# Kernel tuning notes

Measured on AMD Instinct MI355X. Metric: run time of the kernel, lower is better.

The kernel has to match this reference:

```python
import jax, jax.numpy as jnp
import numpy as np

D_MODEL = 1024
N_HEADS = 16
HEAD_DIM = D_MODEL // N_HEADS


def setup_inputs() -> dict:
    key = jax.random.key(0)
    k_x, k_qkv, k_out = jax.random.split(key, 3)
    x = jax.random.normal(k_x, (4, 2048, D_MODEL), dtype=jnp.float32)
    # nn.Linear weights are (out_features, in_features); init std=0.02
    w_qkv = jax.random.normal(k_qkv, (3 * D_MODEL, D_MODEL), dtype=jnp.float32) * 0.02
    w_out = jax.random.normal(k_out, (D_MODEL, D_MODEL), dtype=jnp.float32) * 0.02
    return {"x": x, "w_qkv": w_qkv, "w_out": w_out}


def reference(x, w_qkv, w_out):
    B, T, C = x.shape
    H, Dh = N_HEADS, HEAD_DIM
    # qkv projection: x @ w_qkv.T -> (B, T, 3C)
    qkv = jnp.einsum('btc,oc->bto', x, w_qkv)
    q, k, v = jnp.split(qkv, 3, axis=-1)

    def split_heads(t):
        return t.reshape(B, T, H, Dh).transpose(0, 2, 1, 3)  # (B, H, T, Dh)

    q, k, v = split_heads(q), split_heads(k), split_heads(v)
    scale = jnp.sqrt(jnp.asarray(Dh, dtype=x.dtype))
    scores = jnp.einsum('bhqd,bhkd->bhqk', q, k) / scale  # (B, H, T, T)
    causal = jnp.tril(jnp.ones((T, T), dtype=bool))
    scores = jnp.where(causal[None, None], scores, jnp.asarray(-jnp.inf, dtype=scores.dtype))
    attn = jax.nn.softmax(scores, axis=-1)
    out = jnp.einsum('bhqk,bhkd->bhqd', attn, v)  # (B, H, T, Dh)
    out = out.transpose(0, 2, 1, 3).reshape(B, T, C)
    return jnp.einsum('btc,oc->bto', out, w_out)
```

## Files before the change

kernel.cpp:

```cpp
#include <hip/hip_runtime.h>

typedef __attribute__((ext_vector_type(8))) short bf16x8;
typedef __attribute__((ext_vector_type(4))) float f32x4;
typedef __attribute__((ext_vector_type(16))) float f32x16;
typedef __attribute__((ext_vector_type(4))) int i32x4;
using u16 = unsigned short;

constexpr int Bsz = 4, T = 2048, C = 1024, H = 16, Dh = 64;
constexpr int Mrows = Bsz * T;
constexpr int K_DIM = 1024;
constexpr float QSCALE = 0.18033688011112042f;

__device__ inline u16 f2bf(float f) {
    unsigned u = __builtin_bit_cast(unsigned, f);
    u += 0x7FFFu + ((u >> 16) & 1u);
    return (u16)(u >> 16);
}

__device__ inline void g2l16(const void* g, void* l) {
    __builtin_amdgcn_global_load_lds((const __attribute__((address_space(1))) void*)g,
                                     (__attribute__((address_space(3))) void*)l, 16, 0, 0);
}

__device__ inline unsigned pk2(float lo, float hi) {
    unsigned d;
    asm("v_cvt_pk_bf16_f32 %0, %1, %2" : "=v"(d) : "v"(lo), "v"(hi));
    return d;
}
__device__ inline void swap32(unsigned& a, unsigned& b) {
    asm("v_permlane32_swap_b32 %0, %1" : "+v"(a), "+v"(b));
}

__global__ __launch_bounds__(256)
void cvt_k(const float* __restrict__ x, const float* __restrict__ wq,
           const float* __restrict__ wo, u16* __restrict__ xb,
           u16* __restrict__ wqb, u16* __restrict__ wob)
{
    int idx = blockIdx.x * 256 + threadIdx.x;
    const float* src; u16* dst; int rel;
    if (idx < 1048576)      { src = x;  dst = xb;  rel = idx; }
    else if (idx < 1441792) { src = wq; dst = wqb; rel = idx - 1048576; }
    else                    { src = wo; dst = wob; rel = idx - 1441792; }
    size_t off = (size_t)rel * 8;
    float4 a = *(const float4*)(src + off);
    float4 b = *(const float4*)(src + off + 4);
    unsigned r0 = (unsigned)f2bf(a.x) | ((unsigned)f2bf(a.y) << 16);
    unsigned r1 = (unsigned)f2bf(a.z) | ((unsigned)f2bf(a.w) << 16);
    unsigned r2 = (unsigned)f2bf(b.x) | ((unsigned)f2bf(b.y) << 16);
    unsigned r3 = (unsigned)f2bf(b.z) | ((unsigned)f2bf(b.w) << 16);
    *(uint4*)(dst + off) = make_uint4(r0, r1, r2, r3);
}

__device__ inline void stage_g(u16* lds, const u16* gb, int ldg, int tid) {
    #pragma unroll
    for (int i = 0; i < 4; ++i) {
        int ch = i * 256 + tid;
        int r = ch >> 3, c8 = ch & 7;
        int sc = c8 ^ (r & 7);
        g2l16(gb + (size_t)r * ldg + sc * 8, lds + (i * 256 + (tid & 192)) * 8);
    }
}

template<int MODE>
__device__ __forceinline__
void gemm_body(const u16* __restrict__ Ab, const u16* __restrict__ Bb,
               float* __restrict__ Op, u16* __restrict__ qws,
               u16* __restrict__ kws, u16* __restrict__ vtws,
               u16* As, u16* Bs, int m0, int n0)
{
    const int tid = threadIdx.x;
    const int l = tid & 63, wid = tid >> 6;
    const int wm = wid >> 1, wn = wid & 1;
    const int lane16 = l & 15, lhi = l >> 4;

    const u16* Abase = Ab + (size_t)m0 * K_DIM;
    const u16* Bbase = Bb + (size_t)n0 * K_DIM;

    f32x4 acc[4][4] = {};

    for (int ks = 0; ks < K_DIM / 64; ++ks) {
        __syncthreads();
        stage_g(As, Abase + ks * 64, K_DIM, tid);
        stage_g(Bs, Bbase + ks * 64, K_DIM, tid);
        __syncthreads();
        #pragma unroll
        for (int kc = 0; kc < 2; kc++) {
            bf16x8 af[4], bfr[4];
            #pragma unroll
            for (int mi = 0; mi < 4; mi++) {
                int row = wm * 64 + mi * 16 + lane16;
                int byte = row * 128 + kc * 64 + lhi * 16; byte ^= (row & 7) << 4;
                af[mi] = *(const bf16x8*)((const char*)As + byte);
            }
            #pragma unroll
            for (int ni = 0; ni < 4; ni++) {
                int row = wn * 64 + ni * 16 + lane16;
                int byte = row * 128 + kc * 64 + lhi * 16; byte ^= (row & 7) << 4;
                bfr[ni] = *(const bf16x8*)((const char*)Bs + byte);
            }
            #pragma unroll
            for (int mi = 0; mi < 4; mi++)
                #pragma unroll
                for (int ni = 0; ni < 4; ni++) {
                    if constexpr (MODE == 2)
                        acc[mi][ni] = __builtin_amdgcn_mfma_f32_16x16x32_bf16(
                            bfr[ni], af[mi], acc[mi][ni], 0, 0, 0);
                    else
                        acc[mi][ni] = __builtin_amdgcn_mfma_f32_16x16x32_bf16(
                            af[mi], bfr[ni], acc[mi][ni], 0, 0, 0);
                }
        }
    }

    if constexpr (MODE == 2) {
        #pragma unroll
        for (int mi = 0; mi < 4; mi++)
            #pragma unroll
            for (int ni = 0; ni < 4; ni++)
                #pragma unroll
                for (int r = 0; r < 4; r++) {
                    int wr = n0 + wn * 64 + ni * 16 + lhi * 4 + r;
                    int tg = m0 + wm * 64 + mi * 16 + lane16;
                    int hh = (wr >> 6) & 15, d = wr & 63;
                    int bb = tg >> 11, tt = tg & 2047;
                    size_t off = (((size_t)bb * H + hh) * Dh + d) * T + tt;
                    vtws[off] = f2bf(acc[mi][ni][r]);
                }
    } else {
        #pragma unroll
        for (int mi = 0; mi < 4; mi++)
            #pragma unroll
            for (int ni = 0; ni < 4; ni++)
                #pragma unroll
                for (int r = 0; r < 4; r++) {
                    int gm = m0 + wm * 64 + mi * 16 + lhi * 4 + r;
                    int gn = n0 + wn * 64 + ni * 16 + lane16;
                    float val = acc[mi][ni][r];
                    if constexpr (MODE == 0) {
                        int hh = (gn >> 6) & 15, d = gn & 63;
                        int bb = gm >> 11, t = gm & 2047;
                        size_t off = (((size_t)bb * H + hh) * T + t) * Dh + d;
                        if (gn < C) qws[off] = f2bf(val * QSCALE);
                        else        kws[off] = f2bf(val);
                    } else {
                        Op[(size_t)gm * C + gn] = val;
                    }
                }
    }
}

__global__ __launch_bounds__(256)
void gemm_qkv(const u16* __restrict__ xb, const u16* __restrict__ wqkvb,
              u16* __restrict__ qws, u16* __restrict__ kws, u16* __restrict__ vtws)
{
    __shared__ alignas(16) u16 As[128 * 64];
    __shared__ alignas(16) u16 Bs[128 * 64];
    const int m0 = blockIdx.x * 128;
    if (blockIdx.y < 16)
        gemm_body<0>(xb, wqkvb, nullptr, qws, kws, vtws, As, Bs, m0, blockIdx.y * 128);
    else
        gemm_body<2>(xb, wqkvb, nullptr, qws, kws, vtws, As, Bs, m0,
                     2 * C + (blockIdx.y - 16) * 128);
}

__global__ __launch_bounds__(256)
void gemm_out(const u16* __restrict__ ob, const u16* __restrict__ woutb,
              float* __restrict__ Op)
{
    __shared__ alignas(16) u16 As[128 * 64];
    __shared__ alignas(16) u16 Bs[128 * 64];
    gemm_body<1>(ob, woutb, Op, nullptr, nullptr, nullptr, As, Bs,
                 blockIdx.x * 128, blockIdx.y * 128);
}

constexpr float SMAX = 16.0f;

__device__ inline void stage_c(u16* lds, const u16* gb, int rstride, int tid) {
    #pragma unroll
    for (int it = 0; it < 2; ++it) {
        int i = it * 256 + tid;
        int r = i & 63, c8 = i >> 6;
        g2l16(gb + (size_t)r * rstride + c8 * 8, lds + i * 8);
    }
}

__global__ __launch_bounds__(256, 3)
void attn_k(const u16* __restrict__ qws, const u16* __restrict__ kws,
            const u16* __restrict__ vtws, u16* __restrict__ ows)
{
    __shared__ alignas(16) u16 KL[3][64 * 64];
    __shared__ alignas(16) u16 VL[3][64 * 64];

    const int bid = blockIdx.x;
    const int head = bid & 63;
    const int qt = 15 - (bid >> 6);
    const int b = head >> 4, h = head & 15;
    const int tid = threadIdx.x, w = tid >> 6, l = tid & 63;
    const int l31 = l & 31, hi = l >> 5;

    const size_t hoff = (size_t)head * (T * Dh);
    const u16* Qg  = qws + hoff;
    const u16* Kg  = kws + hoff;
    const u16* Vtg = vtws + hoff;

    const int qb = qt * 128;
    const int nt = 2 * qt + 2;
    const int qbw = qb + w * 32;

    bf16x8 qf[4];
    #pragma unroll
    for (int c = 0; c < 4; ++c)
        qf[c] = *(const bf16x8*)(Qg + (size_t)(qbw + l31) * Dh + c * 16 + hi * 8);

    f32x16 o0{}, o1{};
    float lrun = 0.f;

    stage_c(KL[0], Kg, Dh, tid);
    stage_c(VL[0], Vtg, T, tid);
    stage_c(KL[1], Kg + (size_t)64 * Dh, Dh, tid);
    stage_c(VL[1], Vtg + 64, T, tid);

    int cur = 0;
    for (int t = 0; t < nt; ++t) {
        if (t + 1 < nt) asm volatile("s_waitcnt vmcnt(4)" ::: "memory");
        else            asm volatile("s_waitcnt vmcnt(0)" ::: "memory");
        __builtin_amdgcn_s_barrier();
        __builtin_amdgcn_sched_barrier(0);

        int nx = cur + 2; if (nx >= 3) nx -= 3;
        if (t + 2 < nt) {
            stage_c(KL[nx], Kg + (size_t)(t + 2) * 64 * Dh, Dh, tid);
            stage_c(VL[nx], Vtg + (t + 2) * 64, T, tid);
        }

        const int kv0 = t * 64;
        if (kv0 <= qbw + 31) {
            const char* Kb = (const char*)KL[cur];
            const char* Vb = (const char*)VL[cur];

            bf16x8 kf0[4], kf1[4];
            #pragma unroll
            for (int c = 0; c < 4; ++c) {
                int off = (c * 2 + hi) * 1024 + l31 * 16;
                kf0[c] = *(const bf16x8*)(Kb + off);
                kf1[c] = *(const bf16x8*)(Kb + off + 512);
            }

            f32x16 s0{}, s1{};
            #pragma unroll
            for (int c = 0; c < 4; ++c) {
                s0 = __builtin_amdgcn_mfma_f32_32x32x16_bf16(kf0[c], qf[c], s0, 0, 0, 0);
                s1 = __builtin_amdgcn_mfma_f32_32x32x16_bf16(kf1[c], qf[c], s1, 0, 0, 0);
            }

            if (kv0 + 63 > qbw) {
                int qg = qbw + l31;
                #pragma unroll
                for (int r = 0; r < 16; ++r) {
                    int kvg = kv0 + (r & 3) + 8 * (r >> 2) + 4 * hi;
                    if (kvg > qg)      s0[r] = -__builtin_inff();
                    if (kvg + 32 > qg) s1[r] = -__builtin_inff();
                }
            }

            float p0[16], p1[16];
            float t0 = 0.f, t1 = 0.f, t2 = 0.f, t3 = 0.f;
            #pragma unroll
            for (int r = 0; r < 16; ++r) {
                p0[r] = __builtin_amdgcn_exp2f(s0[r] - SMAX);
                p1[r] = __builtin_amdgcn_exp2f(s1[r] - SMAX);
                float s = p0[r] + p1[r];
                if ((r & 3) == 0) t0 += s; else if ((r & 3) == 1) t1 += s;
                else if ((r & 3) == 2) t2 += s; else t3 += s;
            }
            lrun += (t0 + t1) + (t2 + t3);

            unsigned paf[4][4];
            unsigned cc[8];
            #pragma unroll
            for (int i = 0; i < 4; ++i) cc[i]     = pk2(p0[2 * i], p0[2 * i + 1]);
            #pragma unroll
            for (int i = 0; i < 4; ++i) cc[4 + i] = pk2(p0[8 + 2 * i], p0[9 + 2 * i]);
            swap32(cc[0], cc[2]); swap32(cc[1], cc[3]);
            swap32(cc[4], cc[6]); swap32(cc[5], cc[7]);
            #pragma unroll
            for (int i = 0; i < 4; ++i) { paf[0][i] = cc[i]; paf[1][i] = cc[4 + i]; }
            #pragma unroll
            for (int i = 0; i < 4; ++i) cc[i]     = pk2(p1[2 * i], p1[2 * i + 1]);
            #pragma unroll
            for (int i = 0; i < 4; ++i) cc[4 + i] = pk2(p1[8 + 2 * i], p1[9 + 2 * i]);
            swap32(cc[0], cc[2]); swap32(cc[1], cc[3]);
            swap32(cc[4], cc[6]); swap32(cc[5], cc[7]);
            #pragma unroll
            for (int i = 0; i < 4; ++i) { paf[2][i] = cc[i]; paf[3][i] = cc[4 + i]; }

            #pragma unroll
            for (int kb = 0; kb < 4; ++kb) {
                i32x4 wv = {(int)paf[kb][0], (int)paf[kb][1],
                            (int)paf[kb][2], (int)paf[kb][3]};
                bf16x8 pa = __builtin_bit_cast(bf16x8, wv);
                int off = (kb * 2 + hi) * 1024 + l31 * 16;
                bf16x8 v0 = *(const bf16x8*)(Vb + off);
                bf16x8 v1 = *(const bf16x8*)(Vb + off + 512);
                o0 = __builtin_amdgcn_mfma_f32_32x32x16_bf16(pa, v0, o0, 0, 0, 0);
                o1 = __builtin_amdgcn_mfma_f32_32x32x16_bf16(pa, v1, o1, 0, 0, 0);
            }
        }
        cur = (cur == 2) ? 0 : cur + 1;
    }

    float lt = lrun + __shfl_xor(lrun, 32);
    float inv = 1.0f / lt;
    #pragma unroll
    for (int r = 0; r < 16; ++r) {
        int cr = (r & 3) + 8 * (r >> 2) + 4 * hi;
        float il = __shfl(inv, cr);
        size_t rowoff = ((size_t)b * T + qb + w * 32 + cr) * C + h * Dh + l31;
        ows[rowoff]      = f2bf(o0[r] * il);
        ows[rowoff + 32] = f2bf(o1[r] * il);
    }
}

extern "C" void kernel_launch(void* const* d_in, const int* in_sizes, int n_in,
                              void* d_out, int out_size, void* d_ws, size_t ws_size,
                              hipStream_t stream)
{
    const float* x     = (const float*)d_in[0];
    const float* w_qkv = (const float*)d_in[1];
    const float* w_out = (const float*)d_in[2];
    float* out = (float*)d_out;

    const size_t SZ = (size_t)Bsz * H * T * Dh;
    u16* qws   = (u16*)d_ws;
    u16* kws   = qws + SZ;
    u16* vtws  = kws + SZ;
    u16* xb    = vtws + SZ;
    u16* ows   = xb;
    u16* wqkvb = xb + SZ;
    u16* woutb = wqkvb + (size_t)3 * C * C;

    cvt_k<<<dim3(6144), 256, 0, stream>>>(x, w_qkv, w_out, xb, wqkvb, woutb);

    gemm_qkv<<<dim3(Mrows / 128, 24), 256, 0, stream>>>(xb, wqkvb, qws, kws, vtws);

    attn_k<<<dim3(1024), 256, 0, stream>>>(qws, kws, vtws, ows);

    gemm_out<<<dim3(Mrows / 128, C / 128), 256, 0, stream>>>(ows, woutb, out);
}
```

Before: 156.9 us.

## Double-buffer GEMM LDS tiles and raise wave priority around attention MFMAs

The QKV and output-projection GEMMs now use two LDS buffers per operand. The next k-slice is prefetched into one buffer while MFMAs run on the other, with a single waitcnt+barrier per iteration instead of two syncthreads. In the attention kernel, s_setprio(1) is placed around the QK and PV MFMA blocks so waves issuing matrix ops get scheduling priority. LDS per GEMM block doubles to 64KB, which may reduce occupancy.

```diff
diff --git a/kernel.cpp b/kernel.cpp
--- a/kernel.cpp
+++ b/kernel.cpp
@@ -66,7 +66,7 @@
 void gemm_body(const u16* __restrict__ Ab, const u16* __restrict__ Bb,
                float* __restrict__ Op, u16* __restrict__ qws,
                u16* __restrict__ kws, u16* __restrict__ vtws,
-               u16* As, u16* Bs, int m0, int n0)
+               u16 (*As)[128 * 64], u16 (*Bs)[128 * 64], int m0, int n0)
 {
     const int tid = threadIdx.x;
     const int l = tid & 63, wid = tid >> 6;
@@ -78,11 +78,18 @@
 
     f32x4 acc[4][4] = {};
 
+    stage_g(As[0], Abase, K_DIM, tid);
+    stage_g(Bs[0], Bbase, K_DIM, tid);
+    asm volatile("s_waitcnt vmcnt(0)" ::: "memory");
+    __builtin_amdgcn_s_barrier();
+    __builtin_amdgcn_sched_barrier(0);
+
     for (int ks = 0; ks < K_DIM / 64; ++ks) {
-        __syncthreads();
-        stage_g(As, Abase + ks * 64, K_DIM, tid);
-        stage_g(Bs, Bbase + ks * 64, K_DIM, tid);
-        __syncthreads();
+        const int cur = ks & 1;
+        if (ks + 1 < K_DIM / 64) {
+            stage_g(As[cur ^ 1], Abase + (ks + 1) * 64, K_DIM, tid);
+            stage_g(Bs[cur ^ 1], Bbase + (ks + 1) * 64, K_DIM, tid);
+        }
         #pragma unroll
         for (int kc = 0; kc < 2; kc++) {
             bf16x8 af[4], bfr[4];
@@ -90,13 +97,13 @@
             for (int mi = 0; mi < 4; mi++) {
                 int row = wm * 64 + mi * 16 + lane16;
                 int byte = row * 128 + kc * 64 + lhi * 16; byte ^= (row & 7) << 4;
-                af[mi] = *(const bf16x8*)((const char*)As + byte);
+                af[mi] = *(const bf16x8*)((const char*)As[cur] + byte);
             }
             #pragma unroll
             for (int ni = 0; ni < 4; ni++) {
                 int row = wn * 64 + ni * 16 + lane16;
                 int byte = row * 128 + kc * 64 + lhi * 16; byte ^= (row & 7) << 4;
-                bfr[ni] = *(const bf16x8*)((const char*)Bs + byte);
+                bfr[ni] = *(const bf16x8*)((const char*)Bs[cur] + byte);
             }
             #pragma unroll
             for (int mi = 0; mi < 4; mi++)
@@ -110,6 +117,9 @@
                             af[mi], bfr[ni], acc[mi][ni], 0, 0, 0);
                 }
         }
+        asm volatile("s_waitcnt vmcnt(0)" ::: "memory");
+        __builtin_amdgcn_s_barrier();
+        __builtin_amdgcn_sched_barrier(0);
     }
 
     if constexpr (MODE == 2) {
@@ -153,8 +163,8 @@
 void gemm_qkv(const u16* __restrict__ xb, const u16* __restrict__ wqkvb,
               u16* __restrict__ qws, u16* __restrict__ kws, u16* __restrict__ vtws)
 {
-    __shared__ alignas(16) u16 As[128 * 64];
-    __shared__ alignas(16) u16 Bs[128 * 64];
+    __shared__ alignas(16) u16 As[2][128 * 64];
+    __shared__ alignas(16) u16 Bs[2][128 * 64];
     const int m0 = blockIdx.x * 128;
     if (blockIdx.y < 16)
         gemm_body<0>(xb, wqkvb, nullptr, qws, kws, vtws, As, Bs, m0, blockIdx.y * 128);
@@ -167,8 +177,8 @@
 void gemm_out(const u16* __restrict__ ob, const u16* __restrict__ woutb,
               float* __restrict__ Op)
 {
-    __shared__ alignas(16) u16 As[128 * 64];
-    __shared__ alignas(16) u16 Bs[128 * 64];
+    __shared__ alignas(16) u16 As[2][128 * 64];
+    __shared__ alignas(16) u16 Bs[2][128 * 64];
     gemm_body<1>(ob, woutb, Op, nullptr, nullptr, nullptr, As, Bs,
                  blockIdx.x * 128, blockIdx.y * 128);
 }
@@ -247,11 +257,13 @@
             }
 
             f32x16 s0{}, s1{};
+            __builtin_amdgcn_s_setprio(1);
             #pragma unroll
             for (int c = 0; c < 4; ++c) {
                 s0 = __builtin_amdgcn_mfma_f32_32x32x16_bf16(kf0[c], qf[c], s0, 0, 0, 0);
                 s1 = __builtin_amdgcn_mfma_f32_32x32x16_bf16(kf1[c], qf[c], s1, 0, 0, 0);
             }
+            __builtin_amdgcn_s_setprio(0);
 
             if (kv0 + 63 > qbw) {
                 int qg = qbw + l31;
@@ -294,6 +306,7 @@
             #pragma unroll
             for (int i = 0; i < 4; ++i) { paf[2][i] = cc[i]; paf[3][i] = cc[4 + i]; }
 
+            __builtin_amdgcn_s_setprio(1);
             #pragma unroll
             for (int kb = 0; kb < 4; ++kb) {
                 i32x4 wv = {(int)paf[kb][0], (int)paf[kb][1],
@@ -305,6 +318,7 @@
                 o0 = __builtin_amdgcn_mfma_f32_32x32x16_bf16(pa, v0, o0, 0, 0, 0);
                 o1 = __builtin_amdgcn_mfma_f32_32x32x16_bf16(pa, v1, o1, 0, 0, 0);
             }
+            __builtin_amdgcn_s_setprio(0);
         }
         cur = (cur == 2) ? 0 : cur + 1;
     }
```

Measured after the change: 172.8 us. 10.1% more time.
